# Kernel optimization log

Hardware: AMD Instinct MI355X
Metric: run time of the kernel (lower is better)

The kernel has to match this reference:

```python
import jax, jax.numpy as jnp
import numpy as np

N = 20000      # nodes
E = 640000     # edges (avg degree 32)
K = 4          # eigenvectors (sign-invariant batch axis)
HID = 64       # hidden_dim
EDIM = 32      # edge_dim == GINE out_channels
ODIM = 64      # out_dim of rho
EPS = 0.0      # GINEConv eps (default, not learned here)


def setup_inputs() -> dict:
    key = jax.random.key(0)
    ks = jax.random.split(key, 20)
    def g(i, shape):
        return jax.random.normal(ks[i], shape, dtype=jnp.float32) / np.float32(np.sqrt(shape[0]))
    inp = {}
    inp["x"] = jax.random.normal(ks[0], (K, N, 1), dtype=jnp.float32)
    inp["edge_attr"] = jax.random.normal(ks[1], (E, EDIM), dtype=jnp.float32)
    inp["edge_index"] = jax.random.randint(ks[2], (2, E), 0, N, dtype=jnp.int32)
    in_dims = [1, HID, HID]
    out_dims = [HID, HID, EDIM]
    i = 3
    for l in range(3):
        inp[f"l{l}_We"] = g(i, (EDIM, in_dims[l])); i += 1
        inp[f"l{l}_be"] = jnp.zeros((in_dims[l],), jnp.float32)
        inp[f"l{l}_W1"] = g(i, (in_dims[l], HID)); i += 1
        inp[f"l{l}_b1"] = jnp.zeros((HID,), jnp.float32)
        inp[f"l{l}_W2"] = g(i, (HID, out_dims[l])); i += 1
        inp[f"l{l}_b2"] = jnp.zeros((out_dims[l],), jnp.float32)
    inp["Wr1"] = g(i, (EDIM, HID)); i += 1
    inp["br1"] = jnp.zeros((HID,), jnp.float32)
    inp["Wr2"] = g(i, (HID, ODIM)); i += 1
    inp["br2"] = jnp.zeros((ODIM,), jnp.float32)
    return inp


def _gine_conv(h, src, dst, edge_attr, We, be, W1, b1, W2, b2):
    # h: [K, N, F_in]; edge linear maps edge features into node feature space
    e_emb = edge_attr @ We + be                      # [E, F_in]
    msg = jax.nn.relu(h[:, src, :] + e_emb)          # [K, E, F_in] gather
    agg = jax.vmap(lambda m: jax.ops.segment_sum(m, dst, num_segments=N))(msg)  # [K, N, F_in] scatter-add
    z = (1.0 + EPS) * h + agg
    return jax.nn.relu(z @ W1 + b1) @ W2 + b2        # per-layer MLP


def _phi(h, src, dst, edge_attr, layers):
    n = len(layers)
    for l, p in enumerate(layers):
        h = _gine_conv(h, src, dst, edge_attr, *p)
        if l < n - 1:
            h = jax.nn.relu(h)
    return h  # [K, N, EDIM]


def reference(x, edge_attr, edge_index,
              l0_We, l0_be, l0_W1, l0_b1, l0_W2, l0_b2,
              l1_We, l1_be, l1_W1, l1_b1, l1_W2, l1_b2,
              l2_We, l2_be, l2_W1, l2_b1, l2_W2, l2_b2,
              Wr1, br1, Wr2, br2):
    src = edge_index[0]
    dst = edge_index[1]
    layers = [
        (l0_We, l0_be, l0_W1, l0_b1, l0_W2, l0_b2),
        (l1_We, l1_be, l1_W1, l1_b1, l1_W2, l1_b2),
        (l2_We, l2_be, l2_W1, l2_b1, l2_W2, l2_b2),
    ]
    # sign invariance: phi(x) + phi(-x)
    phi_out = _phi(x, src, dst, edge_attr, layers) + _phi(-x, src, dst, edge_attr, layers)
    pooled = jnp.sum(phi_out, axis=0)                # sum over K eigenvectors -> [N, EDIM]
    return jax.nn.relu(pooled @ Wr1 + br1) @ Wr2 + br2  # rho MLP -> [N, ODIM]
```

## Files before the change

### kernel.cpp

```cpp
#include <hip/hip_runtime.h>

#define NN 20000
#define NE 640000
#define NCH 8
#define HID 64
#define EDIM 32
#define ODIM 64

typedef __attribute__((ext_vector_type(8))) short bf16x8;
typedef __attribute__((ext_vector_type(4))) float f32x4;

__device__ __forceinline__ float b2f(unsigned short u) {
    unsigned v = ((unsigned)u) << 16;
    return __builtin_bit_cast(float, v);
}
__device__ __forceinline__ unsigned short f2b(float f) {
    unsigned u = __builtin_bit_cast(unsigned, f);
    unsigned r = (u + 0x7fffu + ((u >> 16) & 1u)) >> 16;
    return (unsigned short)r;
}
__device__ __forceinline__ f32x4 mfma16(bf16x8 a, bf16x8 b, f32x4 c) {
    return __builtin_amdgcn_mfma_f32_16x16x32_bf16(a, b, c, 0, 0, 0);
}
__device__ __forceinline__ bf16x8 load_bfrag(const unsigned short* W, int ldn, int k0, int n0, int lane) {
    int g = lane >> 4, r = lane & 15;
    bf16x8 f;
#pragma unroll
    for (int j = 0; j < 8; ++j) f[j] = (short)W[(k0 + 8 * g + j) * ldn + n0 + r];
    return f;
}

__global__ __launch_bounds__(256) void k_prep(
    const float* We1, const float* We2, const float* W11, const float* W21,
    const float* W12, const float* W22, const float* W20, const float* Wr1,
    const float* Wr2, unsigned short* bw)
{
    int gid = blockIdx.x * 256 + threadIdx.x;
    const float* src; int off;
    if      (gid < 2048)  { src = We1; off = 0; }
    else if (gid < 4096)  { src = We2; off = 2048; }
    else if (gid < 8192)  { src = W11; off = 4096; }
    else if (gid < 12288) { src = W21; off = 8192; }
    else if (gid < 16384) { src = W12; off = 12288; }
    else if (gid < 18432) { src = W22; off = 16384; }
    else if (gid < 22528) { src = W20; off = 18432; }
    else if (gid < 24576) { src = Wr1; off = 22528; }
    else                  { src = Wr2; off = 24576; }
    bw[gid] = f2b(src[gid - off]);
}

__global__ __launch_bounds__(256) void k_hist(const int* __restrict__ ei, int* __restrict__ cnt,
                                              const float* __restrict__ x, float* __restrict__ xt)
{
    int e = blockIdx.x * 256 + threadIdx.x;
    if (e < NE) atomicAdd(&cnt[ei[NE + e]], 1);
    if (e < NN) {
        f32x4 v = {x[e], x[NN + e], x[2 * NN + e], x[3 * NN + e]};
        *(f32x4*)(xt + (size_t)e * 4) = v;
    }
}

__global__ __launch_bounds__(1024) void k_scan(const int* __restrict__ cnt,
                                               int* __restrict__ row, int* __restrict__ cursor)
{
    __shared__ int part[1024];
    int t = threadIdx.x;
    int base = t * 20;
    int s = 0;
#pragma unroll
    for (int i = 0; i < 20; ++i) { int idx = base + i; if (idx < NN) s += cnt[idx]; }
    part[t] = s;
    __syncthreads();
    int v = s;
    for (int off = 1; off < 1024; off <<= 1) {
        int add = (t >= off) ? part[t - off] : 0;
        __syncthreads();
        v += add;
        part[t] = v;
        __syncthreads();
    }
    int run = v - s;
    for (int i = 0; i < 20; ++i) {
        int idx = base + i;
        if (idx < NN) { row[idx] = run; cursor[idx] = run; run += cnt[idx]; }
    }
    if (t == 1023) row[NN] = NE;
}

__global__ __launch_bounds__(256) void k_scatter2(
    const int* __restrict__ ei, int* __restrict__ cursor,
    const float* __restrict__ ea, const float* __restrict__ We0, const float* __restrict__ be0,
    int* __restrict__ srcp, unsigned short* __restrict__ eap, float* __restrict__ emb0)
{
    int e = blockIdx.x * 256 + threadIdx.x;
    if (e >= NE) return;
    int d = ei[NE + e];
    int pos = atomicAdd(&cursor[d], 1);
    srcp[pos] = ei[e];
    const f32x4* s4 = (const f32x4*)(ea + (size_t)e * 32);
    float e0 = be0[0];
#pragma unroll
    for (int h = 0; h < 4; ++h) {
        f32x4 a = s4[2 * h], b = s4[2 * h + 1];
        bf16x8 o;
#pragma unroll
        for (int j = 0; j < 4; ++j) {
            e0 = fmaf(a[j], We0[h * 8 + j], e0);
            e0 = fmaf(b[j], We0[h * 8 + 4 + j], e0);
            o[j] = (short)f2b(a[j]);
            o[4 + j] = (short)f2b(b[j]);
        }
        *(bf16x8*)(eap + (size_t)pos * 32 + h * 8) = o;
    }
    emb0[pos] = e0;
}

__global__ __launch_bounds__(256) void k_l0_gather(
    const float* __restrict__ xt, const int* __restrict__ srcp,
    const int* __restrict__ row, const float* __restrict__ emb0,
    float* __restrict__ z0)
{
    int gwave = (blockIdx.x * 256 + threadIdx.x) >> 6;
    int half = (threadIdx.x >> 5) & 1;
    int l = threadIdx.x & 31;
    int d = gwave * 2 + half;
    if (d >= NN) return;
    int p0 = row[d], p1 = row[d + 1];
    float ap0 = 0.f, ap1 = 0.f, ap2 = 0.f, ap3 = 0.f;
    float am0 = 0.f, am1 = 0.f, am2 = 0.f, am3 = 0.f;
    for (int p = p0 + l; p < p1; p += 32) {
        float e0 = emb0[p];
        f32x4 xs = *(const f32x4*)(xt + (size_t)srcp[p] * 4);
        ap0 += fmaxf(xs[0] + e0, 0.f); am0 += fmaxf(e0 - xs[0], 0.f);
        ap1 += fmaxf(xs[1] + e0, 0.f); am1 += fmaxf(e0 - xs[1], 0.f);
        ap2 += fmaxf(xs[2] + e0, 0.f); am2 += fmaxf(e0 - xs[2], 0.f);
        ap3 += fmaxf(xs[3] + e0, 0.f); am3 += fmaxf(e0 - xs[3], 0.f);
    }
#pragma unroll
    for (int off = 1; off < 32; off <<= 1) {
        ap0 += __shfl_xor(ap0, off, 64); am0 += __shfl_xor(am0, off, 64);
        ap1 += __shfl_xor(ap1, off, 64); am1 += __shfl_xor(am1, off, 64);
        ap2 += __shfl_xor(ap2, off, 64); am2 += __shfl_xor(am2, off, 64);
        ap3 += __shfl_xor(ap3, off, 64); am3 += __shfl_xor(am3, off, 64);
    }
    if (l == 0) {
        f32x4 xd = *(const f32x4*)(xt + (size_t)d * 4);
        f32x4 zp = {xd[0] + ap0, xd[1] + ap1, xd[2] + ap2, xd[3] + ap3};
        f32x4 zm = {am0 - xd[0], am1 - xd[1], am2 - xd[2], am3 - xd[3]};
        *(f32x4*)(z0 + (size_t)d * 8) = zp;
        *(f32x4*)(z0 + (size_t)d * 8 + 4) = zm;
    }
}

__global__ __launch_bounds__(256) void k_l0_mlp(
    const float* __restrict__ z0,
    const float* __restrict__ W1, const float* __restrict__ b1,
    const unsigned short* __restrict__ W2b, const float* __restrict__ b2,
    unsigned short* __restrict__ hT)
{
    constexpr int S = 72;
    __shared__ short lds[4][16 * S];
    int lane = threadIdx.x & 63, wid = threadIdx.x >> 6, g = lane >> 4, r = lane & 15;
    short* L = lds[wid];
    bf16x8 w2f[2][4];
#pragma unroll
    for (int kk = 0; kk < 2; ++kk)
#pragma unroll
        for (int t = 0; t < 4; ++t) w2f[kk][t] = load_bfrag(W2b, 64, kk * 32, t * 16, lane);
    float b2v[4];
#pragma unroll
    for (int t = 0; t < 4; ++t) b2v[t] = b2[t * 16 + r];
    float w1a[8], w1b[8], b1a[8], b1b[8];
#pragma unroll
    for (int j = 0; j < 8; ++j) {
        w1a[j] = W1[8 * g + j];      b1a[j] = b1[8 * g + j];
        w1b[j] = W1[32 + 8 * g + j]; b1b[j] = b1[32 + 8 * g + j];
    }
    int tile = blockIdx.x * 4 + wid;
    int row0 = tile * 16;
    float zv = z0[row0 + r];
    bf16x8 a0, a1;
#pragma unroll
    for (int j = 0; j < 8; ++j) {
        a0[j] = (short)f2b(fmaxf(fmaf(zv, w1a[j], b1a[j]), 0.f));
        a1[j] = (short)f2b(fmaxf(fmaf(zv, w1b[j], b1b[j]), 0.f));
    }
    f32x4 c2[4];
#pragma unroll
    for (int t = 0; t < 4; ++t) {
        f32x4 c = {0.f, 0.f, 0.f, 0.f};
        c = mfma16(a0, w2f[0][t], c);
        c = mfma16(a1, w2f[1][t], c);
        c2[t] = c;
    }
#pragma unroll
    for (int t = 0; t < 4; ++t)
#pragma unroll
        for (int i = 0; i < 4; ++i)
            L[(4 * g + i) * S + t * 16 + r] = (short)f2b(fmaxf(c2[t][i] + b2v[t], 0.f));
    asm volatile("" ::: "memory");
    int node0 = tile * 2;
#pragma unroll
    for (int half = 0; half < 2; ++half) {
        bf16x8 v;
#pragma unroll
        for (int c = 0; c < 8; ++c) v[c] = L[(half * 8 + c) * S + lane];
        *(bf16x8*)(hT + (size_t)(node0 + half) * 512 + lane * 8) = v;
    }
}

__global__ __launch_bounds__(256) void k_gather_f(
    const int* __restrict__ srcp, const int* __restrict__ row,
    const unsigned short* __restrict__ eap,
    const unsigned short* __restrict__ Web, const float* __restrict__ be,
    const unsigned short* __restrict__ hT, unsigned short* __restrict__ z)
{
    constexpr int SE = 66;
    __shared__ short Lw[4 * 64 * 8];
    __shared__ short Lem[4][16 * SE];
    int lane = threadIdx.x & 63, wid = threadIdx.x >> 6, g = lane >> 4, r = lane & 15;
    short* Le = Lem[wid];

    {
        bf16x8 f = load_bfrag(Web, 64, 0, wid * 16, lane);
        *(bf16x8*)(Lw + (wid * 64 + lane) * 8) = f;
    }
    float bev[4];
#pragma unroll
    for (int t = 0; t < 4; ++t) bev[t] = be[t * 16 + r];
    __syncthreads();

    int d = blockIdx.x * 4 + wid;
    int p0 = row[d], p1 = row[d + 1];
    float acc[NCH];
#pragma unroll
    for (int c = 0; c < NCH; ++c) acc[c] = 0.f;

    for (int p = p0; p < p1; p += 16) {
        int ne = p1 - p; if (ne > 16) ne = 16;
        int pp = p + r; if (pp > p1 - 1) pp = p1 - 1;
        bf16x8 afc = *(const bf16x8*)(eap + (size_t)pp * 32 + 8 * g);
        int svc = srcp[pp];
#pragma unroll
        for (int t = 0; t < 4; ++t) {
            bf16x8 wfrag = *(const bf16x8*)(Lw + (t * 64 + lane) * 8);
            f32x4 cc = {bev[t], bev[t], bev[t], bev[t]};
            cc = mfma16(afc, wfrag, cc);
#pragma unroll
            for (int i = 0; i < 4; ++i) {
                unsigned short v = (4 * g + i < ne) ? f2b(cc[i]) : (unsigned short)0xFF80;
                Le[(4 * g + i) * SE + t * 16 + r] = (short)v;
            }
        }
        asm volatile("" ::: "memory");
#pragma unroll
        for (int b = 0; b < 4; ++b) {
#pragma unroll
            for (int q = 4 * b; q < 4 * b + 4; ++q) {
                int src = __builtin_amdgcn_readlane(svc, q);
                float em = b2f((unsigned short)Le[q * SE + lane]);
                uint4 hv = *(const uint4*)(hT + (size_t)src * 512 + (lane << 3));
                acc[0] += fmaxf(__builtin_bit_cast(float, hv.x << 16) + em, 0.f);
                acc[1] += fmaxf(__builtin_bit_cast(float, hv.x & 0xffff0000u) + em, 0.f);
                acc[2] += fmaxf(__builtin_bit_cast(float, hv.y << 16) + em, 0.f);
                acc[3] += fmaxf(__builtin_bit_cast(float, hv.y & 0xffff0000u) + em, 0.f);
                acc[4] += fmaxf(__builtin_bit_cast(float, hv.z << 16) + em, 0.f);
                acc[5] += fmaxf(__builtin_bit_cast(float, hv.z & 0xffff0000u) + em, 0.f);
                acc[6] += fmaxf(__builtin_bit_cast(float, hv.w << 16) + em, 0.f);
                acc[7] += fmaxf(__builtin_bit_cast(float, hv.w & 0xffff0000u) + em, 0.f);
            }
            __builtin_amdgcn_sched_barrier(0);
        }
        asm volatile("" ::: "memory");
    }

    uint4 hd = *(const uint4*)(hT + (size_t)d * 512 + (lane << 3));
    unsigned hw[4] = {hd.x, hd.y, hd.z, hd.w};
    unsigned short* zd = z + (size_t)d * 8 * 64 + lane;
#pragma unroll
    for (int j = 0; j < 4; ++j) {
        float lo = __builtin_bit_cast(float, hw[j] << 16);
        float hi = __builtin_bit_cast(float, hw[j] & 0xffff0000u);
        zd[(2 * j) * 64] = f2b(lo + acc[2 * j]);
        zd[(2 * j + 1) * 64] = f2b(hi + acc[2 * j + 1]);
    }
}

template <int OUT, bool RELU2, bool TOHT>
__global__ __launch_bounds__(256) void k_mlp(
    const unsigned short* __restrict__ z,
    const unsigned short* __restrict__ W1b, const float* __restrict__ b1,
    const unsigned short* __restrict__ W2b, const float* __restrict__ b2,
    unsigned short* __restrict__ hout)
{
    constexpr int S1 = 72;
    constexpr int S2 = (OUT == 64) ? 72 : 40;
    constexpr int NT2 = OUT / 16;
    __shared__ short lds[4][16 * S1];
    int lane = threadIdx.x & 63, wid = threadIdx.x >> 6, g = lane >> 4, r = lane & 15;
    short* L = lds[wid];

    bf16x8 w1f[2][4];
#pragma unroll
    for (int kk = 0; kk < 2; ++kk)
#pragma unroll
        for (int t = 0; t < 4; ++t) w1f[kk][t] = load_bfrag(W1b, 64, kk * 32, t * 16, lane);
    bf16x8 w2f[2][NT2];
#pragma unroll
    for (int kk = 0; kk < 2; ++kk)
#pragma unroll
        for (int t = 0; t < NT2; ++t) w2f[kk][t] = load_bfrag(W2b, OUT, kk * 32, t * 16, lane);
    float b1v[4], b2v[NT2];
#pragma unroll
    for (int t = 0; t < 4; ++t) b1v[t] = b1[t * 16 + r];
#pragma unroll
    for (int t = 0; t < NT2; ++t) b2v[t] = b2[t * 16 + r];

    int tile = blockIdx.x * 4 + wid;
    int row0 = tile * 16;

    bf16x8 a0 = *(const bf16x8*)(z + (size_t)(row0 + r) * 64 + 8 * g);
    bf16x8 a1 = *(const bf16x8*)(z + (size_t)(row0 + r) * 64 + 32 + 8 * g);
    f32x4 c1[4];
#pragma unroll
    for (int t = 0; t < 4; ++t) {
        f32x4 c = {0.f, 0.f, 0.f, 0.f};
        c = mfma16(a0, w1f[0][t], c);
        c = mfma16(a1, w1f[1][t], c);
        c1[t] = c;
    }
#pragma unroll
    for (int t = 0; t < 4; ++t)
#pragma unroll
        for (int i = 0; i < 4; ++i)
            L[(4 * g + i) * S1 + t * 16 + r] = (short)f2b(fmaxf(c1[t][i] + b1v[t], 0.f));
    asm volatile("" ::: "memory");
    bf16x8 t0 = *(const bf16x8*)(L + r * S1 + 8 * g);
    bf16x8 t1 = *(const bf16x8*)(L + r * S1 + 32 + 8 * g);
    f32x4 c2[NT2];
#pragma unroll
    for (int t = 0; t < NT2; ++t) {
        f32x4 c = {0.f, 0.f, 0.f, 0.f};
        c = mfma16(t0, w2f[0][t], c);
        c = mfma16(t1, w2f[1][t], c);
        c2[t] = c;
    }
    asm volatile("" ::: "memory");
#pragma unroll
    for (int t = 0; t < NT2; ++t)
#pragma unroll
        for (int i = 0; i < 4; ++i) {
            float v = c2[t][i] + b2v[t];
            if (RELU2) v = fmaxf(v, 0.f);
            L[(4 * g + i) * S2 + t * 16 + r] = (short)f2b(v);
        }
    asm volatile("" ::: "memory");
    if (TOHT) {
        int node0 = tile * 2;
#pragma unroll
        for (int half = 0; half < 2; ++half) {
            bf16x8 v;
#pragma unroll
            for (int c = 0; c < 8; ++c) v[c] = L[(half * 8 + c) * S2 + lane];
            *(bf16x8*)(hout + (size_t)(node0 + half) * 512 + lane * 8) = v;
        }
    } else {
        bf16x8 o0 = *(const bf16x8*)(L + r * S2 + 8 * g);
        *(bf16x8*)(hout + (size_t)(row0 + r) * OUT + 8 * g) = o0;
    }
}

__global__ __launch_bounds__(256) void k_rho(
    const unsigned short* __restrict__ h2,
    const unsigned short* __restrict__ Wr1b, const float* __restrict__ br1,
    const unsigned short* __restrict__ Wr2b, const float* __restrict__ br2,
    float* __restrict__ out)
{
    constexpr int S = 72;
    __shared__ short lds[4][16 * S];
    int lane = threadIdx.x & 63, wid = threadIdx.x >> 6, g = lane >> 4, r = lane & 15;
    short* L = lds[wid];
    int tile = blockIdx.x * 4 + wid;
    if (tile * 16 >= NN) return;
    bf16x8 w1f[4], w2f[2][4];
#pragma unroll
    for (int t = 0; t < 4; ++t) w1f[t] = load_bfrag(Wr1b, 64, 0, t * 16, lane);
#pragma unroll
    for (int kk = 0; kk < 2; ++kk)
#pragma unroll
        for (int t = 0; t < 4; ++t) w2f[kk][t] = load_bfrag(Wr2b, 64, kk * 32, t * 16, lane);
    float b1v[4], b2v[4];
#pragma unroll
    for (int t = 0; t < 4; ++t) { b1v[t] = br1[t * 16 + r]; b2v[t] = br2[t * 16 + r]; }

    int n = tile * 16 + r;
    float s[8] = {0.f, 0.f, 0.f, 0.f, 0.f, 0.f, 0.f, 0.f};
#pragma unroll
    for (int c = 0; c < NCH; ++c) {
        bf16x8 hv = *(const bf16x8*)(h2 + ((size_t)n * 8 + c) * 32 + 8 * g);
#pragma unroll
        for (int j = 0; j < 8; ++j) s[j] += b2f((unsigned short)hv[j]);
    }
    bf16x8 af;
#pragma unroll
    for (int j = 0; j < 8; ++j) af[j] = (short)f2b(s[j]);
    f32x4 c1[4];
#pragma unroll
    for (int t = 0; t < 4; ++t) {
        f32x4 c = {0.f, 0.f, 0.f, 0.f};
        c1[t] = mfma16(af, w1f[t], c);
    }
#pragma unroll
    for (int t = 0; t < 4; ++t)
#pragma unroll
        for (int i = 0; i < 4; ++i)
            L[(4 * g + i) * S + t * 16 + r] = (short)f2b(fmaxf(c1[t][i] + b1v[t], 0.f));
    asm volatile("" ::: "memory");
    bf16x8 t0 = *(const bf16x8*)(L + r * S + 8 * g);
    bf16x8 t1 = *(const bf16x8*)(L + r * S + 32 + 8 * g);
    f32x4 c2[4];
#pragma unroll
    for (int t = 0; t < 4; ++t) {
        f32x4 c = {0.f, 0.f, 0.f, 0.f};
        c = mfma16(t0, w2f[0][t], c);
        c = mfma16(t1, w2f[1][t], c);
        c2[t] = c;
    }
    int nb = tile * 16;
#pragma unroll
    for (int t = 0; t < 4; ++t)
#pragma unroll
        for (int i = 0; i < 4; ++i)
            out[(size_t)(nb + 4 * g + i) * 64 + t * 16 + r] = c2[t][i] + b2v[t];
}

extern "C" void kernel_launch(void* const* d_in, const int* in_sizes, int n_in,
                              void* d_out, int out_size, void* d_ws, size_t ws_size,
                              hipStream_t stream)
{
    const float* x   = (const float*)d_in[0];
    const float* ea  = (const float*)d_in[1];
    const int*   ei  = (const int*)d_in[2];
    const float* We0 = (const float*)d_in[3];
    const float* be0 = (const float*)d_in[4];
    const float* W10 = (const float*)d_in[5];
    const float* b10 = (const float*)d_in[6];
    const float* W20 = (const float*)d_in[7];
    const float* b20 = (const float*)d_in[8];
    const float* We1 = (const float*)d_in[9];
    const float* be1 = (const float*)d_in[10];
    const float* W11 = (const float*)d_in[11];
    const float* b11 = (const float*)d_in[12];
    const float* W21 = (const float*)d_in[13];
    const float* b21 = (const float*)d_in[14];
    const float* We2 = (const float*)d_in[15];
    const float* be2 = (const float*)d_in[16];
    const float* W12 = (const float*)d_in[17];
    const float* b12 = (const float*)d_in[18];
    const float* W22 = (const float*)d_in[19];
    const float* b22 = (const float*)d_in[20];
    const float* Wr1 = (const float*)d_in[21];
    const float* br1 = (const float*)d_in[22];
    const float* Wr2 = (const float*)d_in[23];
    const float* br2 = (const float*)d_in[24];
    float* out = (float*)d_out;

    char* base = (char*)d_ws;
    unsigned short* hT   = (unsigned short*)base; base += (size_t)NN * 512 * 2;
    unsigned short* z    = (unsigned short*)base; base += (size_t)160000 * 64 * 2;
    unsigned short* h2   = (unsigned short*)base; base += (size_t)160000 * 32 * 2;
    unsigned short* eap  = (unsigned short*)base; base += (size_t)NE * 32 * 2;
    float* emb0          = (float*)base;          base += (size_t)NE * 4;
    float* z0            = (float*)base;          base += (size_t)160000 * 4;
    float* xt            = (float*)base;          base += (size_t)NN * 4 * 4;
    int* srcp            = (int*)base;            base += (size_t)NE * 4;
    int* row             = (int*)base;            base += 80128;
    int* cnt             = (int*)base;            base += 80128;
    int* cursor          = (int*)base;            base += 80128;
    unsigned short* bw   = (unsigned short*)base;

    const unsigned short* bWe1 = bw;
    const unsigned short* bWe2 = bw + 2048;
    const unsigned short* bW11 = bw + 4096;
    const unsigned short* bW21 = bw + 8192;
    const unsigned short* bW12 = bw + 12288;
    const unsigned short* bW22 = bw + 16384;
    const unsigned short* bW20 = bw + 18432;
    const unsigned short* bWr1 = bw + 22528;
    const unsigned short* bWr2 = bw + 24576;

    k_prep<<<112, 256, 0, stream>>>(We1, We2, W11, W21, W12, W22, W20, Wr1, Wr2, bw);
    hipMemsetAsync(cnt, 0, NN * sizeof(int), stream);
    k_hist<<<NE / 256, 256, 0, stream>>>(ei, cnt, x, xt);
    k_scan<<<1, 1024, 0, stream>>>(cnt, row, cursor);
    k_scatter2<<<NE / 256, 256, 0, stream>>>(ei, cursor, ea, We0, be0, srcp, eap, emb0);

    k_l0_gather<<<(NN / 2 + 3) / 4, 256, 0, stream>>>(xt, srcp, row, emb0, z0);
    k_l0_mlp<<<2500, 256, 0, stream>>>(z0, W10, b10, bW20, b20, hT);

    k_gather_f<<<NN / 4, 256, 0, stream>>>(srcp, row, eap, bWe1, be1, hT, z);
    k_mlp<64, true, true><<<2500, 256, 0, stream>>>(z, bW11, b11, bW21, b21, hT);

    k_gather_f<<<NN / 4, 256, 0, stream>>>(srcp, row, eap, bWe2, be2, hT, z);
    k_mlp<32, false, false><<<2500, 256, 0, stream>>>(z, bW12, b12, bW22, b22, h2);

    k_rho<<<313, 256, 0, stream>>>(h2, bWr1, br1, bWr2, br2, out);
}
```

Measured before the change: 358.1 us.

## Fuse prep with histogram, layer-0 gather with MLP, and final MLP with rho

Three kernel pairs become one kernel each. Weight conversion moves into the histogram kernel. The layer-0 gather hands its 16 z values to the MLP through shared memory instead of a global z0 buffer. The last layer's MLP now sums the 8 sign/eigenvector channels in LDS and runs the rho MLP in place, which removes the h2 buffer and its round trip. This cuts launch count and intermediate global traffic, at the cost of extra register pressure and some idle lanes in the rho stage (only 2 of 16 rows are active).

```diff
diff --git a/kernel.cpp b/kernel.cpp
--- a/kernel.cpp
+++ b/kernel.cpp
@@ -30,33 +30,31 @@
     return f;
 }
 
-__global__ __launch_bounds__(256) void k_prep(
+__global__ __launch_bounds__(256) void k_prep_hist(
     const float* We1, const float* We2, const float* W11, const float* W21,
     const float* W12, const float* W22, const float* W20, const float* Wr1,
-    const float* Wr2, unsigned short* bw)
+    const float* Wr2, unsigned short* bw,
+    const int* __restrict__ ei, int* __restrict__ cnt,
+    const float* __restrict__ x, float* __restrict__ xt)
 {
     int gid = blockIdx.x * 256 + threadIdx.x;
-    const float* src; int off;
-    if      (gid < 2048)  { src = We1; off = 0; }
-    else if (gid < 4096)  { src = We2; off = 2048; }
-    else if (gid < 8192)  { src = W11; off = 4096; }
-    else if (gid < 12288) { src = W21; off = 8192; }
-    else if (gid < 16384) { src = W12; off = 12288; }
-    else if (gid < 18432) { src = W22; off = 16384; }
-    else if (gid < 22528) { src = W20; off = 18432; }
-    else if (gid < 24576) { src = Wr1; off = 22528; }
-    else                  { src = Wr2; off = 24576; }
-    bw[gid] = f2b(src[gid - off]);
-}
-
-__global__ __launch_bounds__(256) void k_hist(const int* __restrict__ ei, int* __restrict__ cnt,
-                                              const float* __restrict__ x, float* __restrict__ xt)
-{
-    int e = blockIdx.x * 256 + threadIdx.x;
-    if (e < NE) atomicAdd(&cnt[ei[NE + e]], 1);
-    if (e < NN) {
-        f32x4 v = {x[e], x[NN + e], x[2 * NN + e], x[3 * NN + e]};
-        *(f32x4*)(xt + (size_t)e * 4) = v;
+    if (gid < NE) atomicAdd(&cnt[ei[NE + gid]], 1);
+    if (gid < NN) {
+        f32x4 v = {x[gid], x[NN + gid], x[2 * NN + gid], x[3 * NN + gid]};
+        *(f32x4*)(xt + (size_t)gid * 4) = v;
+    }
+    if (gid < 28672) {
+        const float* src; int off;
+        if      (gid < 2048)  { src = We1; off = 0; }
+        else if (gid < 4096)  { src = We2; off = 2048; }
+        else if (gid < 8192)  { src = W11; off = 4096; }
+        else if (gid < 12288) { src = W21; off = 8192; }
+        else if (gid < 16384) { src = W12; off = 12288; }
+        else if (gid < 18432) { src = W22; off = 16384; }
+        else if (gid < 22528) { src = W20; off = 18432; }
+        else if (gid < 24576) { src = Wr1; off = 22528; }
+        else                  { src = Wr2; off = 24576; }
+        bw[gid] = f2b(src[gid - off]);
     }
 }
 
@@ -115,16 +113,21 @@
     emb0[pos] = e0;
 }
 
-__global__ __launch_bounds__(256) void k_l0_gather(
+__global__ __launch_bounds__(256) void k_l0_fused(
     const float* __restrict__ xt, const int* __restrict__ srcp,
     const int* __restrict__ row, const float* __restrict__ emb0,
-    float* __restrict__ z0)
-{
-    int gwave = (blockIdx.x * 256 + threadIdx.x) >> 6;
-    int half = (threadIdx.x >> 5) & 1;
-    int l = threadIdx.x & 31;
-    int d = gwave * 2 + half;
-    if (d >= NN) return;
+    const float* __restrict__ W1, const float* __restrict__ b1,
+    const unsigned short* __restrict__ W2b, const float* __restrict__ b2,
+    unsigned short* __restrict__ hT)
+{
+    constexpr int S = 72;
+    __shared__ float zrow[4][16];
+    __shared__ short lds[4][16 * S];
+    int lane = threadIdx.x & 63, wid = threadIdx.x >> 6, g = lane >> 4, r = lane & 15;
+    int gw = blockIdx.x * 4 + wid;
+    int halfq = lane >> 5, l = lane & 31;
+    int d = gw * 2 + halfq;
+
     int p0 = row[d], p1 = row[d + 1];
     float ap0 = 0.f, ap1 = 0.f, ap2 = 0.f, ap3 = 0.f;
     float am0 = 0.f, am1 = 0.f, am2 = 0.f, am3 = 0.f;
@@ -145,22 +148,19 @@
     }
     if (l == 0) {
         f32x4 xd = *(const f32x4*)(xt + (size_t)d * 4);
-        f32x4 zp = {xd[0] + ap0, xd[1] + ap1, xd[2] + ap2, xd[3] + ap3};
-        f32x4 zm = {am0 - xd[0], am1 - xd[1], am2 - xd[2], am3 - xd[3]};
-        *(f32x4*)(z0 + (size_t)d * 8) = zp;
-        *(f32x4*)(z0 + (size_t)d * 8 + 4) = zm;
-    }
-}
-
-__global__ __launch_bounds__(256) void k_l0_mlp(
-    const float* __restrict__ z0,
-    const float* __restrict__ W1, const float* __restrict__ b1,
-    const unsigned short* __restrict__ W2b, const float* __restrict__ b2,
-    unsigned short* __restrict__ hT)
-{
-    constexpr int S = 72;
-    __shared__ short lds[4][16 * S];
-    int lane = threadIdx.x & 63, wid = threadIdx.x >> 6, g = lane >> 4, r = lane & 15;
+        zrow[wid][halfq * 8 + 0] = xd[0] + ap0;
+        zrow[wid][halfq * 8 + 1] = xd[1] + ap1;
+        zrow[wid][halfq * 8 + 2] = xd[2] + ap2;
+        zrow[wid][halfq * 8 + 3] = xd[3] + ap3;
+        zrow[wid][halfq * 8 + 4] = am0 - xd[0];
+        zrow[wid][halfq * 8 + 5] = am1 - xd[1];
+        zrow[wid][halfq * 8 + 6] = am2 - xd[2];
+        zrow[wid][halfq * 8 + 7] = am3 - xd[3];
+    }
+    asm volatile("" ::: "memory");
+    __builtin_amdgcn_sched_barrier(0);
+
+    float zv = zrow[wid][r];
     short* L = lds[wid];
     bf16x8 w2f[2][4];
 #pragma unroll
@@ -176,9 +176,6 @@
         w1a[j] = W1[8 * g + j];      b1a[j] = b1[8 * g + j];
         w1b[j] = W1[32 + 8 * g + j]; b1b[j] = b1[32 + 8 * g + j];
     }
-    int tile = blockIdx.x * 4 + wid;
-    int row0 = tile * 16;
-    float zv = z0[row0 + r];
     bf16x8 a0, a1;
 #pragma unroll
     for (int j = 0; j < 8; ++j) {
@@ -199,7 +196,7 @@
         for (int i = 0; i < 4; ++i)
             L[(4 * g + i) * S + t * 16 + r] = (short)f2b(fmaxf(c2[t][i] + b2v[t], 0.f));
     asm volatile("" ::: "memory");
-    int node0 = tile * 2;
+    int node0 = gw * 2;
 #pragma unroll
     for (int half = 0; half < 2; ++half) {
         bf16x8 v;
@@ -286,35 +283,28 @@
     }
 }
 
-template <int OUT, bool RELU2, bool TOHT>
-__global__ __launch_bounds__(256) void k_mlp(
+__global__ __launch_bounds__(256) void k_mlp64(
     const unsigned short* __restrict__ z,
     const unsigned short* __restrict__ W1b, const float* __restrict__ b1,
     const unsigned short* __restrict__ W2b, const float* __restrict__ b2,
     unsigned short* __restrict__ hout)
 {
     constexpr int S1 = 72;
-    constexpr int S2 = (OUT == 64) ? 72 : 40;
-    constexpr int NT2 = OUT / 16;
     __shared__ short lds[4][16 * S1];
     int lane = threadIdx.x & 63, wid = threadIdx.x >> 6, g = lane >> 4, r = lane & 15;
     short* L = lds[wid];
 
-    bf16x8 w1f[2][4];
+    bf16x8 w1f[2][4], w2f[2][4];
 #pragma unroll
     for (int kk = 0; kk < 2; ++kk)
 #pragma unroll
-        for (int t = 0; t < 4; ++t) w1f[kk][t] = load_bfrag(W1b, 64, kk * 32, t * 16, lane);
-    bf16x8 w2f[2][NT2];
-#pragma unroll
-    for (int kk = 0; kk < 2; ++kk)
-#pragma unroll
-        for (int t = 0; t < NT2; ++t) w2f[kk][t] = load_bfrag(W2b, OUT, kk * 32, t * 16, lane);
-    float b1v[4], b2v[NT2];
-#pragma unroll
-    for (int t = 0; t < 4; ++t) b1v[t] = b1[t * 16 + r];
-#pragma unroll
-    for (int t = 0; t < NT2; ++t) b2v[t] = b2[t * 16 + r];
+        for (int t = 0; t < 4; ++t) {
+            w1f[kk][t] = load_bfrag(W1b, 64, kk * 32, t * 16, lane);
+            w2f[kk][t] = load_bfrag(W2b, 64, kk * 32, t * 16, lane);
+        }
+    float b1v[4], b2v[4];
+#pragma unroll
+    for (int t = 0; t < 4; ++t) { b1v[t] = b1[t * 16 + r]; b2v[t] = b2[t * 16 + r]; }
 
     int tile = blockIdx.x * 4 + wid;
     int row0 = tile * 16;
@@ -337,87 +327,6 @@
     asm volatile("" ::: "memory");
     bf16x8 t0 = *(const bf16x8*)(L + r * S1 + 8 * g);
     bf16x8 t1 = *(const bf16x8*)(L + r * S1 + 32 + 8 * g);
-    f32x4 c2[NT2];
-#pragma unroll
-    for (int t = 0; t < NT2; ++t) {
-        f32x4 c = {0.f, 0.f, 0.f, 0.f};
-        c = mfma16(t0, w2f[0][t], c);
-        c = mfma16(t1, w2f[1][t], c);
-        c2[t] = c;
-    }
-    asm volatile("" ::: "memory");
-#pragma unroll
-    for (int t = 0; t < NT2; ++t)
-#pragma unroll
-        for (int i = 0; i < 4; ++i) {
-            float v = c2[t][i] + b2v[t];
-            if (RELU2) v = fmaxf(v, 0.f);
-            L[(4 * g + i) * S2 + t * 16 + r] = (short)f2b(v);
-        }
-    asm volatile("" ::: "memory");
-    if (TOHT) {
-        int node0 = tile * 2;
-#pragma unroll
-        for (int half = 0; half < 2; ++half) {
-            bf16x8 v;
-#pragma unroll
-            for (int c = 0; c < 8; ++c) v[c] = L[(half * 8 + c) * S2 + lane];
-            *(bf16x8*)(hout + (size_t)(node0 + half) * 512 + lane * 8) = v;
-        }
-    } else {
-        bf16x8 o0 = *(const bf16x8*)(L + r * S2 + 8 * g);
-        *(bf16x8*)(hout + (size_t)(row0 + r) * OUT + 8 * g) = o0;
-    }
-}
-
-__global__ __launch_bounds__(256) void k_rho(
-    const unsigned short* __restrict__ h2,
-    const unsigned short* __restrict__ Wr1b, const float* __restrict__ br1,
-    const unsigned short* __restrict__ Wr2b, const float* __restrict__ br2,
-    float* __restrict__ out)
-{
-    constexpr int S = 72;
-    __shared__ short lds[4][16 * S];
-    int lane = threadIdx.x & 63, wid = threadIdx.x >> 6, g = lane >> 4, r = lane & 15;
-    short* L = lds[wid];
-    int tile = blockIdx.x * 4 + wid;
-    if (tile * 16 >= NN) return;
-    bf16x8 w1f[4], w2f[2][4];
-#pragma unroll
-    for (int t = 0; t < 4; ++t) w1f[t] = load_bfrag(Wr1b, 64, 0, t * 16, lane);
-#pragma unroll
-    for (int kk = 0; kk < 2; ++kk)
-#pragma unroll
-        for (int t = 0; t < 4; ++t) w2f[kk][t] = load_bfrag(Wr2b, 64, kk * 32, t * 16, lane);
-    float b1v[4], b2v[4];
-#pragma unroll
-    for (int t = 0; t < 4; ++t) { b1v[t] = br1[t * 16 + r]; b2v[t] = br2[t * 16 + r]; }
-
-    int n = tile * 16 + r;
-    float s[8] = {0.f, 0.f, 0.f, 0.f, 0.f, 0.f, 0.f, 0.f};
-#pragma unroll
-    for (int c = 0; c < NCH; ++c) {
-        bf16x8 hv = *(const bf16x8*)(h2 + ((size_t)n * 8 + c) * 32 + 8 * g);
-#pragma unroll
-        for (int j = 0; j < 8; ++j) s[j] += b2f((unsigned short)hv[j]);
-    }
-    bf16x8 af;
-#pragma unroll
-    for (int j = 0; j < 8; ++j) af[j] = (short)f2b(s[j]);
-    f32x4 c1[4];
-#pragma unroll
-    for (int t = 0; t < 4; ++t) {
-        f32x4 c = {0.f, 0.f, 0.f, 0.f};
-        c1[t] = mfma16(af, w1f[t], c);
-    }
-#pragma unroll
-    for (int t = 0; t < 4; ++t)
-#pragma unroll
-        for (int i = 0; i < 4; ++i)
-            L[(4 * g + i) * S + t * 16 + r] = (short)f2b(fmaxf(c1[t][i] + b1v[t], 0.f));
-    asm volatile("" ::: "memory");
-    bf16x8 t0 = *(const bf16x8*)(L + r * S + 8 * g);
-    bf16x8 t1 = *(const bf16x8*)(L + r * S + 32 + 8 * g);
     f32x4 c2[4];
 #pragma unroll
     for (int t = 0; t < 4; ++t) {
@@ -426,12 +335,133 @@
         c = mfma16(t1, w2f[1][t], c);
         c2[t] = c;
     }
-    int nb = tile * 16;
+    asm volatile("" ::: "memory");
 #pragma unroll
     for (int t = 0; t < 4; ++t)
 #pragma unroll
         for (int i = 0; i < 4; ++i)
-            out[(size_t)(nb + 4 * g + i) * 64 + t * 16 + r] = c2[t][i] + b2v[t];
+            L[(4 * g + i) * S1 + t * 16 + r] = (short)f2b(fmaxf(c2[t][i] + b2v[t], 0.f));
+    asm volatile("" ::: "memory");
+    int node0 = tile * 2;
+#pragma unroll
+    for (int half = 0; half < 2; ++half) {
+        bf16x8 v;
+#pragma unroll
+        for (int c = 0; c < 8; ++c) v[c] = L[(half * 8 + c) * S1 + lane];
+        *(bf16x8*)(hout + (size_t)(node0 + half) * 512 + lane * 8) = v;
+    }
+}
+
+__global__ __launch_bounds__(256) void k_mlp_rho(
+    const unsigned short* __restrict__ z,
+    const unsigned short* __restrict__ W1b, const float* __restrict__ b1,
+    const unsigned short* __restrict__ W2b, const float* __restrict__ b2,
+    const unsigned short* __restrict__ Wr1b, const float* __restrict__ br1,
+    const unsigned short* __restrict__ Wr2b, const float* __restrict__ br2,
+    float* __restrict__ out)
+{
+    constexpr int S1 = 72, S2 = 40;
+    __shared__ short lds[4][16 * S1];
+    int lane = threadIdx.x & 63, wid = threadIdx.x >> 6, g = lane >> 4, r = lane & 15;
+    short* L = lds[wid];
+
+    bf16x8 w1f[2][4], w2f[2][2];
+#pragma unroll
+    for (int kk = 0; kk < 2; ++kk) {
+#pragma unroll
+        for (int t = 0; t < 4; ++t) w1f[kk][t] = load_bfrag(W1b, 64, kk * 32, t * 16, lane);
+#pragma unroll
+        for (int t = 0; t < 2; ++t) w2f[kk][t] = load_bfrag(W2b, 32, kk * 32, t * 16, lane);
+    }
+    float b1v[4], b2v[2];
+#pragma unroll
+    for (int t = 0; t < 4; ++t) b1v[t] = b1[t * 16 + r];
+#pragma unroll
+    for (int t = 0; t < 2; ++t) b2v[t] = b2[t * 16 + r];
+
+    int tile = blockIdx.x * 4 + wid;
+    int row0 = tile * 16;
+
+    bf16x8 a0 = *(const bf16x8*)(z + (size_t)(row0 + r) * 64 + 8 * g);
+    bf16x8 a1 = *(const bf16x8*)(z + (size_t)(row0 + r) * 64 + 32 + 8 * g);
+    f32x4 c1[4];
+#pragma unroll
+    for (int t = 0; t < 4; ++t) {
+        f32x4 c = {0.f, 0.f, 0.f, 0.f};
+        c = mfma16(a0, w1f[0][t], c);
+        c = mfma16(a1, w1f[1][t], c);
+        c1[t] = c;
+    }
+#pragma unroll
+    for (int t = 0; t < 4; ++t)
+#pragma unroll
+        for (int i = 0; i < 4; ++i)
+            L[(4 * g + i) * S1 + t * 16 + r] = (short)f2b(fmaxf(c1[t][i] + b1v[t], 0.f));
+    asm volatile("" ::: "memory");
+    bf16x8 t0 = *(const bf16x8*)(L + r * S1 + 8 * g);
+    bf16x8 t1 = *(const bf16x8*)(L + r * S1 + 32 + 8 * g);
+    f32x4 c2[2];
+#pragma unroll
+    for (int t = 0; t < 2; ++t) {
+        f32x4 c = {0.f, 0.f, 0.f, 0.f};
+        c = mfma16(t0, w2f[0][t], c);
+        c = mfma16(t1, w2f[1][t], c);
+        c2[t] = c;
+    }
+    asm volatile("" ::: "memory");
+#pragma unroll
+    for (int t = 0; t < 2; ++t)
+#pragma unroll
+        for (int i = 0; i < 4; ++i)
+            L[(4 * g + i) * S2 + t * 16 + r] = (short)f2b(c2[t][i] + b2v[t]);
+    asm volatile("" ::: "memory");
+
+    bf16x8 af = {0, 0, 0, 0, 0, 0, 0, 0};
+    if (r < 2) {
+#pragma unroll
+        for (int j = 0; j < 8; ++j) {
+            float s = 0.f;
+#pragma unroll
+            for (int c = 0; c < 8; ++c) s += b2f((unsigned short)L[(r * 8 + c) * S2 + 8 * g + j]);
+            af[j] = (short)f2b(s);
+        }
+    }
+    asm volatile("" ::: "memory");
+
+    f32x4 c1r[4];
+#pragma unroll
+    for (int t = 0; t < 4; ++t) {
+        bf16x8 wf = load_bfrag(Wr1b, 64, 0, t * 16, lane);
+        float bb = br1[t * 16 + r];
+        f32x4 cc = {bb, bb, bb, bb};
+        c1r[t] = mfma16(af, wf, cc);
+    }
+#pragma unroll
+    for (int t = 0; t < 4; ++t)
+#pragma unroll
+        for (int i = 0; i < 4; ++i)
+            L[(4 * g + i) * S1 + t * 16 + r] = (short)f2b(fmaxf(c1r[t][i], 0.f));
+    asm volatile("" ::: "memory");
+    bf16x8 t0r = *(const bf16x8*)(L + r * S1 + 8 * g);
+    bf16x8 t1r = *(const bf16x8*)(L + r * S1 + 32 + 8 * g);
+    f32x4 c2r[4];
+#pragma unroll
+    for (int t = 0; t < 4; ++t) {
+        float bb = br2[t * 16 + r];
+        f32x4 cc = {bb, bb, bb, bb};
+        cc = mfma16(t0r, load_bfrag(Wr2b, 64, 0, t * 16, lane), cc);
+        cc = mfma16(t1r, load_bfrag(Wr2b, 64, 32, t * 16, lane), cc);
+        c2r[t] = cc;
+    }
+    if (g == 0) {
+        int node0 = tile * 2;
+#pragma unroll
+        for (int t = 0; t < 4; ++t) {
+#pragma unroll
+            for (int i = 0; i < 2; ++i)
+                out[(size_t)(node0 + i) * 64 + t * 16 + r] = c2r[t][i];
+        }
+    }
 }
 
 extern "C" void kernel_launch(void* const* d_in, const int* in_sizes, int n_in,
@@ -468,10 +498,8 @@
     char* base = (char*)d_ws;
     unsigned short* hT   = (unsigned short*)base; base += (size_t)NN * 512 * 2;
     unsigned short* z    = (unsigned short*)base; base += (size_t)160000 * 64 * 2;
-    unsigned short* h2   = (unsigned short*)base; base += (size_t)160000 * 32 * 2;
     unsigned short* eap  = (unsigned short*)base; base += (size_t)NE * 32 * 2;
     float* emb0          = (float*)base;          base += (size_t)NE * 4;
-    float* z0            = (float*)base;          base += (size_t)160000 * 4;
     float* xt            = (float*)base;          base += (size_t)NN * 4 * 4;
     int* srcp            = (int*)base;            base += (size_t)NE * 4;
     int* row             = (int*)base;            base += 80128;
@@ -489,20 +517,17 @@
     const unsigned short* bWr1 = bw + 22528;
     const unsigned short* bWr2 = bw + 24576;
 
-    k_prep<<<112, 256, 0, stream>>>(We1, We2, W11, W21, W12, W22, W20, Wr1, Wr2, bw);
     hipMemsetAsync(cnt, 0, NN * sizeof(int), stream);
-    k_hist<<<NE / 256, 256, 0, stream>>>(ei, cnt, x, xt);
+    k_prep_hist<<<NE / 256, 256, 0, stream>>>(We1, We2, W11, W21, W12, W22, W20, Wr1, Wr2,
+                                              bw, ei, cnt, x, xt);
     k_scan<<<1, 1024, 0, stream>>>(cnt, row, cursor);
     k_scatter2<<<NE / 256, 256, 0, stream>>>(ei, cursor, ea, We0, be0, srcp, eap, emb0);
 
-    k_l0_gather<<<(NN / 2 + 3) / 4, 256, 0, stream>>>(xt, srcp, row, emb0, z0);
-    k_l0_mlp<<<2500, 256, 0, stream>>>(z0, W10, b10, bW20, b20, hT);
+    k_l0_fused<<<2500, 256, 0, stream>>>(xt, srcp, row, emb0, W10, b10, bW20, b20, hT);
 
     k_gather_f<<<NN / 4, 256, 0, stream>>>(srcp, row, eap, bWe1, be1, hT, z);
-    k_mlp<64, true, true><<<2500, 256, 0, stream>>>(z, bW11, b11, bW21, b21, hT);
+    k_mlp64<<<2500, 256, 0, stream>>>(z, bW11, b11, bW21, b21, hT);
 
     k_gather_f<<<NN / 4, 256, 0, stream>>>(srcp, row, eap, bWe2, be2, hT, z);
-    k_mlp<32, false, false><<<2500, 256, 0, stream>>>(z, bW12, b12, bW22, b22, h2);
-
-    k_rho<<<313, 256, 0, stream>>>(h2, bWr1, br1, bWr2, br2, out);
-}
+    k_mlp_rho<<<2500, 256, 0, stream>>>(z, bW12, b12, bW22, b22, bWr1, br1, bWr2, br2, out);
+}
```

Measured after the change: 354.4 us. About the same (-1.0%).
